# Optimization experiments

Hardware: AMD Instinct MI355X
Metric: run time of the kernel (lower is better)

The kernel has to match this reference:

```python
import jax, jax.numpy as jnp
import numpy as np

BN_EPS = 1e-5


def binarize(x):
    # Deterministic sign binarization to {-1, +1} (binarization mode 1).
    return jnp.where(x >= 0, 1.0, -1.0).astype(x.dtype)


def setup_inputs() -> dict:
    key = jax.random.key(0)
    k = jax.random.split(key, 4)
    N, Cin, Cout, H, W, K = 16, 64, 64, 256, 256, 3
    x = jax.random.normal(k[0], (N, Cin, H, W), dtype=jnp.float32)
    w = jax.random.normal(k[1], (Cout, Cin, K, K), dtype=jnp.float32) * 0.1
    b = jax.random.normal(k[2], (Cout,), dtype=jnp.float32) * 0.1
    gamma = jnp.ones((Cout,), dtype=jnp.float32)
    beta = jnp.zeros((Cout,), dtype=jnp.float32)
    running_mean = jax.random.normal(k[3], (Cout,), dtype=jnp.float32) * 0.1
    running_var = jax.random.uniform(jax.random.fold_in(key, 7), (Cout,), dtype=jnp.float32, minval=0.5, maxval=1.5)
    return {"x": x, "w": w, "b": b, "gamma": gamma, "beta": beta,
            "running_mean": running_mean, "running_var": running_var}


def reference(x, w, b, gamma, beta, running_mean, running_var):
    # binarize activations and weights to +-1
    xb = binarize(x)
    wb = binarize(w)
    # 3x3 conv, stride 1, padding 1, dilation 1, NCHW/OIHW
    y = jax.lax.conv_general_dilated(
        xb, wb,
        window_strides=(1, 1),
        padding=((1, 1), (1, 1)),
        dimension_numbers=("NCHW", "OIHW", "NCHW"),
    ) + b[None, :, None, None]
    # ReLU
    y = jnp.maximum(y, 0.0)
    # Dropout2d in eval mode is identity.
    # BatchNorm2d in eval mode: use running stats, affine=True.
    inv = gamma * jax.lax.rsqrt(running_var + BN_EPS)
    y = y * inv[None, :, None, None] + (beta - running_mean * inv)[None, :, None, None]
    return y
```

## Files before the change

kernel.cpp:

```cpp
#include <hip/hip_runtime.h>
#include <stdint.h>

#define NB 16
#define CC 64
#define HH 256
#define WW 256
#define HP 258
#define WP 258

__global__ __launch_bounds__(256) void pack_w_kernel(const float* __restrict__ w,
                                                     uint64_t* __restrict__ pW) {
    int widx = (blockIdx.x * 256 + threadIdx.x) >> 6;
    int lane = threadIdx.x & 63;
    if (widx >= CC * 9) return;
    int o = widx / 9;
    int t = widx % 9;
    float v = w[(size_t)o * (CC * 9) + (size_t)lane * 9 + t];
    unsigned long long m = __ballot(v < 0.0f);
    if (lane == 0) pW[widx] = m;
}

__global__ __launch_bounds__(256) void pack_x_kernel(const float* __restrict__ x,
                                                     uint64_t* __restrict__ pX) {
    int n = blockIdx.y;
    if (blockIdx.x == 0) {
        for (int r = threadIdx.x; r < 1028; r += 256) {
            size_t base = (size_t)n * HP * WP;
            size_t off;
            if (r < 258) off = (size_t)r;
            else if (r < 516) off = (size_t)257 * WP + (r - 258);
            else {
                int rr = r - 516;
                off = (size_t)(1 + (rr >> 1)) * WP + ((rr & 1) ? 257 : 0);
            }
            pX[base + off] = 0;
        }
    }
    int g = blockIdx.x * 256 + threadIdx.x;
    const float4* xv = (const float4*)x;
    uint64_t b0 = 0, b1 = 0, b2 = 0, b3 = 0;
#pragma unroll 16
    for (int c = 0; c < CC; ++c) {
        float4 v = xv[((size_t)(n * CC + c) << 14) + g];
        b0 |= (uint64_t)(v.x < 0.0f) << c;
        b1 |= (uint64_t)(v.y < 0.0f) << c;
        b2 |= (uint64_t)(v.z < 0.0f) << c;
        b3 |= (uint64_t)(v.w < 0.0f) << c;
    }
    int px = g << 2;
    int h = px >> 8;
    int w = px & 255;
    uint64_t* dst = pX + ((size_t)n * HP + (h + 1)) * WP + (w + 1);
    dst[0] = b0; dst[1] = b1; dst[2] = b2; dst[3] = b3;
}

template<bool EDGE>
__device__ __forceinline__ void conv_rows(const uint64_t (*__restrict__ sq)[10],
                                          const int4 (*__restrict__ siv)[2],
                                          const float4* __restrict__ sfv,
                                          const uint64_t xw[3][6],
                                          bool isT, bool isB, bool isL, bool isR,
                                          float4* __restrict__ out4, size_t obase) {
#pragma unroll 2
    for (int o = 0; o < CC; ++o) {
        const ulonglong2* qp = (const ulonglong2*)(&sq[o][0]);
        ulonglong2 q01 = qp[0], q23 = qp[1], q45 = qp[2], q67 = qp[3], q8p = qp[4];
        uint64_t q0 = q01.x, q1 = q01.y, q2 = q23.x, q3 = q23.y, q4 = q45.x,
                 q5 = q45.y, q6 = q67.x, q7 = q67.y, q8 = q8p.x;
        float4 ff = sfv[o];
        int4 e0 = siv[o][0];
        int cL = e0.z, cR = e0.w;
        float A;
        if (EDGE) {
            int4 e1 = siv[o][1];
            int hcorr = 0;
            if (isT) { hcorr += e0.x; cL -= e1.x; cR -= e1.y; }
            if (isB) { hcorr += e0.y; cL -= e1.z; cR -= e1.w; }
            A = (float)(576 - hcorr) + ff.x;
        } else {
            A = 576.0f + ff.x;
        }
        float AL = isL ? A - (float)cL : A;
        float AR = isR ? A - (float)cR : A;

        float4 res;
        float* resp = (float*)&res;
#pragma unroll
        for (int j = 0; j < 4; ++j) {
            int p = __popcll(xw[0][j] ^ q0) + __popcll(xw[0][j + 1] ^ q1) + __popcll(xw[0][j + 2] ^ q2)
                  + __popcll(xw[1][j] ^ q3) + __popcll(xw[1][j + 1] ^ q4) + __popcll(xw[1][j + 2] ^ q5)
                  + __popcll(xw[2][j] ^ q6) + __popcll(xw[2][j + 1] ^ q7) + __popcll(xw[2][j + 2] ^ q8);
            float Aj = (j == 0) ? AL : ((j == 3) ? AR : A);
            float yf = fmaf((float)p, -2.0f, Aj);
            yf = fmaxf(yf, 0.0f);
            resp[j] = fmaf(yf, ff.y, ff.z);
        }
        out4[obase + ((size_t)o << 14)] = res;
    }
}

__global__ __launch_bounds__(256, 4) void bconv_kernel(const uint64_t* __restrict__ pX,
                                                       const uint64_t* __restrict__ pW,
                                                       const float* __restrict__ bias,
                                                       const float* __restrict__ gamma,
                                                       const float* __restrict__ beta,
                                                       const float* __restrict__ rmean,
                                                       const float* __restrict__ rvar,
                                                       float* __restrict__ out) {
    __shared__ __align__(16) uint64_t sq[CC][10];
    __shared__ int4 siv[CC][2];
    __shared__ float4 sfv[CC];

    int tid = threadIdx.x;
    if (tid < CC) {
        int o = tid;
        int ct[9];
#pragma unroll
        for (int t = 0; t < 9; ++t) {
            uint64_t q = pW[o * 9 + t];
            sq[o][t] = q;
            ct[t] = 64 - 2 * __popcll(q);
        }
        sq[o][9] = 0;
        siv[o][0] = make_int4(ct[0] + ct[1] + ct[2],
                              ct[6] + ct[7] + ct[8],
                              ct[0] + ct[3] + ct[6],
                              ct[2] + ct[5] + ct[8]);
        siv[o][1] = make_int4(ct[0], ct[2], ct[6], ct[8]);
        float inv = gamma[o] / sqrtf(rvar[o] + 1e-5f);
        sfv[o] = make_float4(bias[o], inv, beta[o] - rmean[o] * inv, 0.0f);
    }

    int blk = blockIdx.x;
    int n = blk >> 6;
    int hq = blk & 63;
    int l = tid & 63;
    int wid = tid >> 6;
    int h = hq * 4 + wid;

    uint64_t xw[3][6];
    const uint64_t* rowp = pX + ((size_t)n * HP + h) * WP + 4 * l;
#pragma unroll
    for (int r = 0; r < 3; ++r) {
        const ulonglong2* p2 = (const ulonglong2*)(rowp + (size_t)r * WP);
        ulonglong2 a = p2[0], b = p2[1], c = p2[2];
        xw[r][0] = a.x; xw[r][1] = a.y; xw[r][2] = b.x;
        xw[r][3] = b.y; xw[r][4] = c.x; xw[r][5] = c.y;
    }

    __syncthreads();

    bool isL = (l == 0), isR = (l == 63);
    bool isT = (h == 0), isB = (h == 255);
    float4* out4 = (float4*)out;
    size_t obase = ((size_t)(n * CC) << 14) + (size_t)h * 64 + l;

    if (hq == 0 || hq == 63) {
        conv_rows<true>(sq, siv, sfv, xw, isT, isB, isL, isR, out4, obase);
    } else {
        conv_rows<false>(sq, siv, sfv, xw, false, false, isL, isR, out4, obase);
    }
}

extern "C" void kernel_launch(void* const* d_in, const int* in_sizes, int n_in,
                              void* d_out, int out_size, void* d_ws, size_t ws_size,
                              hipStream_t stream) {
    const float* x     = (const float*)d_in[0];
    const float* w     = (const float*)d_in[1];
    const float* bias  = (const float*)d_in[2];
    const float* gamma = (const float*)d_in[3];
    const float* beta  = (const float*)d_in[4];
    const float* rmean = (const float*)d_in[5];
    const float* rvar  = (const float*)d_in[6];
    float* out = (float*)d_out;

    uint64_t* pX = (uint64_t*)d_ws;
    size_t pXwords = (size_t)NB * HP * WP;
    uint64_t* pW = pX + pXwords;

    pack_w_kernel<<<(CC * 9 + 3) / 4, 256, 0, stream>>>(w, pW);
    pack_x_kernel<<<dim3(64, NB), 256, 0, stream>>>(x, pX);
    bconv_kernel<<<NB * 64, 256, 0, stream>>>(pX, pW, bias, gamma, beta, rmean, rvar, out);
}
```

Before: 509.5 us.

## Compute 8 pixels per thread and split output channels across a second grid dimension

Each thread now computes 8 adjacent output pixels instead of 4, so loaded packed-input words are reused across more outputs and sliding-window overlap cost is amortized. Blocks shrink to 128 threads covering the same 4 rows, and the grid gains a y dimension that splits the 64 output channels into two halves of 32. This raises register use (xw grows to 30 words) and duplicates input loads across the two channel halves. Each thread now stores two consecutive float4s per channel instead of one.

```diff
diff --git a/kernel.cpp b/kernel.cpp
--- a/kernel.cpp
+++ b/kernel.cpp
@@ -7,6 +7,7 @@
 #define WW 256
 #define HP 258
 #define WP 258
+#define OH 32
 
 __global__ __launch_bounds__(256) void pack_w_kernel(const float* __restrict__ w,
                                                      uint64_t* __restrict__ pW) {
@@ -55,27 +56,27 @@
 }
 
 template<bool EDGE>
-__device__ __forceinline__ void conv_rows(const uint64_t (*__restrict__ sq)[10],
-                                          const int4 (*__restrict__ siv)[2],
-                                          const float4* __restrict__ sfv,
-                                          const uint64_t xw[3][6],
-                                          bool isT, bool isB, bool isL, bool isR,
-                                          float4* __restrict__ out4, size_t obase) {
+__device__ __forceinline__ void conv8(const uint64_t (*__restrict__ sq)[10],
+                                      const int4 (*__restrict__ siv)[2],
+                                      const float4* __restrict__ sfv,
+                                      const uint64_t xw[3][10],
+                                      bool isT, bool isB, bool isL, bool isR,
+                                      float4* __restrict__ out4, size_t ob) {
 #pragma unroll 2
-    for (int o = 0; o < CC; ++o) {
-        const ulonglong2* qp = (const ulonglong2*)(&sq[o][0]);
+    for (int oi = 0; oi < OH; ++oi) {
+        const ulonglong2* qp = (const ulonglong2*)(&sq[oi][0]);
         ulonglong2 q01 = qp[0], q23 = qp[1], q45 = qp[2], q67 = qp[3], q8p = qp[4];
         uint64_t q0 = q01.x, q1 = q01.y, q2 = q23.x, q3 = q23.y, q4 = q45.x,
                  q5 = q45.y, q6 = q67.x, q7 = q67.y, q8 = q8p.x;
-        float4 ff = sfv[o];
-        int4 e0 = siv[o][0];
+        float4 ff = sfv[oi];
+        int4 e0 = siv[oi][0];
         int cL = e0.z, cR = e0.w;
         float A;
         if (EDGE) {
-            int4 e1 = siv[o][1];
-            int hcorr = 0;
-            if (isT) { hcorr += e0.x; cL -= e1.x; cR -= e1.y; }
-            if (isB) { hcorr += e0.y; cL -= e1.z; cR -= e1.w; }
+            int4 e1 = siv[oi][1];
+            int hcorr = (isT ? e0.x : 0) + (isB ? e0.y : 0);
+            cL -= (isT ? e1.x : 0) + (isB ? e1.z : 0);
+            cR -= (isT ? e1.y : 0) + (isB ? e1.w : 0);
             A = (float)(576 - hcorr) + ff.x;
         } else {
             A = 576.0f + ff.x;
@@ -83,23 +84,24 @@
         float AL = isL ? A - (float)cL : A;
         float AR = isR ? A - (float)cR : A;
 
-        float4 res;
-        float* resp = (float*)&res;
+        float res[8];
 #pragma unroll
-        for (int j = 0; j < 4; ++j) {
+        for (int j = 0; j < 8; ++j) {
             int p = __popcll(xw[0][j] ^ q0) + __popcll(xw[0][j + 1] ^ q1) + __popcll(xw[0][j + 2] ^ q2)
                   + __popcll(xw[1][j] ^ q3) + __popcll(xw[1][j + 1] ^ q4) + __popcll(xw[1][j + 2] ^ q5)
                   + __popcll(xw[2][j] ^ q6) + __popcll(xw[2][j + 1] ^ q7) + __popcll(xw[2][j + 2] ^ q8);
-            float Aj = (j == 0) ? AL : ((j == 3) ? AR : A);
+            float Aj = (j == 0) ? AL : ((j == 7) ? AR : A);
             float yf = fmaf((float)p, -2.0f, Aj);
             yf = fmaxf(yf, 0.0f);
-            resp[j] = fmaf(yf, ff.y, ff.z);
+            res[j] = fmaf(yf, ff.y, ff.z);
         }
-        out4[obase + ((size_t)o << 14)] = res;
+        out4[ob]     = make_float4(res[0], res[1], res[2], res[3]);
+        out4[ob + 1] = make_float4(res[4], res[5], res[6], res[7]);
+        ob += (size_t)1 << 14;
     }
 }
 
-__global__ __launch_bounds__(256, 4) void bconv_kernel(const uint64_t* __restrict__ pX,
+__global__ __launch_bounds__(128, 4) void bconv_kernel(const uint64_t* __restrict__ pX,
                                                        const uint64_t* __restrict__ pW,
                                                        const float* __restrict__ bias,
                                                        const float* __restrict__ gamma,
@@ -107,58 +109,62 @@
                                                        const float* __restrict__ rmean,
                                                        const float* __restrict__ rvar,
                                                        float* __restrict__ out) {
-    __shared__ __align__(16) uint64_t sq[CC][10];
-    __shared__ int4 siv[CC][2];
-    __shared__ float4 sfv[CC];
+    __shared__ __align__(16) uint64_t sq[OH][10];
+    __shared__ int4 siv[OH][2];
+    __shared__ float4 sfv[OH];
 
     int tid = threadIdx.x;
-    if (tid < CC) {
-        int o = tid;
+    int ob0 = blockIdx.y * OH;
+    if (tid < OH) {
+        int o = ob0 + tid;
         int ct[9];
 #pragma unroll
         for (int t = 0; t < 9; ++t) {
             uint64_t q = pW[o * 9 + t];
-            sq[o][t] = q;
+            sq[tid][t] = q;
             ct[t] = 64 - 2 * __popcll(q);
         }
-        sq[o][9] = 0;
-        siv[o][0] = make_int4(ct[0] + ct[1] + ct[2],
-                              ct[6] + ct[7] + ct[8],
-                              ct[0] + ct[3] + ct[6],
-                              ct[2] + ct[5] + ct[8]);
-        siv[o][1] = make_int4(ct[0], ct[2], ct[6], ct[8]);
+        sq[tid][9] = 0;
+        siv[tid][0] = make_int4(ct[0] + ct[1] + ct[2],
+                                ct[6] + ct[7] + ct[8],
+                                ct[0] + ct[3] + ct[6],
+                                ct[2] + ct[5] + ct[8]);
+        siv[tid][1] = make_int4(ct[0], ct[2], ct[6], ct[8]);
         float inv = gamma[o] / sqrtf(rvar[o] + 1e-5f);
-        sfv[o] = make_float4(bias[o], inv, beta[o] - rmean[o] * inv, 0.0f);
+        sfv[tid] = make_float4(bias[o], inv, beta[o] - rmean[o] * inv, 0.0f);
     }
 
     int blk = blockIdx.x;
     int n = blk >> 6;
-    int hq = blk & 63;
+    int rg = blk & 63;
     int l = tid & 63;
     int wid = tid >> 6;
-    int h = hq * 4 + wid;
+    int lh = l >> 5;
+    int lw = l & 31;
+    int h = rg * 4 + wid * 2 + lh;
 
-    uint64_t xw[3][6];
-    const uint64_t* rowp = pX + ((size_t)n * HP + h) * WP + 4 * l;
+    uint64_t xw[3][10];
+    const uint64_t* rowp = pX + ((size_t)n * HP + h) * WP + 8 * lw;
 #pragma unroll
     for (int r = 0; r < 3; ++r) {
         const ulonglong2* p2 = (const ulonglong2*)(rowp + (size_t)r * WP);
-        ulonglong2 a = p2[0], b = p2[1], c = p2[2];
-        xw[r][0] = a.x; xw[r][1] = a.y; xw[r][2] = b.x;
-        xw[r][3] = b.y; xw[r][4] = c.x; xw[r][5] = c.y;
+        ulonglong2 a = p2[0], b = p2[1], c = p2[2], d = p2[3], e = p2[4];
+        xw[r][0] = a.x; xw[r][1] = a.y; xw[r][2] = b.x; xw[r][3] = b.y;
+        xw[r][4] = c.x; xw[r][5] = c.y; xw[r][6] = d.x; xw[r][7] = d.y;
+        xw[r][8] = e.x; xw[r][9] = e.y;
     }
 
     __syncthreads();
 
-    bool isL = (l == 0), isR = (l == 63);
+    bool isL = (lw == 0), isR = (lw == 31);
     bool isT = (h == 0), isB = (h == 255);
     float4* out4 = (float4*)out;
-    size_t obase = ((size_t)(n * CC) << 14) + (size_t)h * 64 + l;
+    size_t ob = ((size_t)(n * CC + ob0) << 14) + (size_t)h * 64 + 2 * lw;
 
-    if (hq == 0 || hq == 63) {
-        conv_rows<true>(sq, siv, sfv, xw, isT, isB, isL, isR, out4, obase);
+    if (rg == 0 || rg == 63) {
+        conv8<true>(sq, siv, sfv, xw, isT, isB, isL, isR, out4, ob);
     } else {
-        conv_rows<false>(sq, siv, sfv, xw, false, false, isL, isR, out4, obase);
+        conv8<false>(sq, siv, sfv, xw, false, false, isL, isR, out4, ob);
     }
 }
 
@@ -180,5 +186,5 @@
 
     pack_w_kernel<<<(CC * 9 + 3) / 4, 256, 0, stream>>>(w, pW);
     pack_x_kernel<<<dim3(64, NB), 256, 0, stream>>>(x, pX);
-    bconv_kernel<<<NB * 64, 256, 0, stream>>>(pX, pW, bias, gamma, beta, rmean, rvar, out);
+    bconv_kernel<<<dim3(NB * 64, 2), 128, 0, stream>>>(pX, pW, bias, gamma, beta, rmean, rvar, out);
 }
```

Result: no change. 510.5 us (+0.2%).
